# Optimization experiments

Measured on AMD Instinct MI355X. Metric: run time of the kernel, lower is better.

## Reference

```python
import jax, jax.numpy as jnp
import numpy as np

N_NODES = 20000
N_EDGES = 640000
H = 64            # node_hidden_size
E_FEAT = 16       # edge_features_size
T = 2             # num_prop_rounds


def setup_inputs() -> dict:
    key = jax.random.key(0)
    ks = jax.random.split(key, 10)
    hv = jax.random.normal(ks[0], (N_NODES, H), dtype=jnp.float32)
    e = jax.random.normal(ks[1], (N_EDGES, E_FEAT), dtype=jnp.float32)
    src = jax.random.randint(ks[2], (N_EDGES,), 0, N_NODES, dtype=jnp.int32)
    dst = jax.random.randint(ks[3], (N_EDGES,), 0, N_NODES, dtype=jnp.int32)
    s = 0.1  # param init scale to keep activations in a sane range
    W_msg = jax.random.normal(ks[4], (T, 2 * H + E_FEAT, 2 * H), dtype=jnp.float32) * s
    b_msg = jax.random.normal(ks[5], (T, 2 * H), dtype=jnp.float32) * s
    W_ih = jax.random.normal(ks[6], (T, 3 * H, 2 * H), dtype=jnp.float32) * s
    W_hh = jax.random.normal(ks[7], (T, 3 * H, H), dtype=jnp.float32) * s
    b_ih = jax.random.normal(ks[8], (T, 3 * H), dtype=jnp.float32) * s
    b_hh = jax.random.normal(ks[9], (T, 3 * H), dtype=jnp.float32) * s
    return {"hv": hv, "e": e, "src": src, "dst": dst,
            "W_msg": W_msg, "b_msg": b_msg,
            "W_ih": W_ih, "W_hh": W_hh, "b_ih": b_ih, "b_hh": b_hh}


def _gru_cell(a, h, W_ih, W_hh, b_ih, b_hh):
    # torch.nn.GRUCell math
    gi = a @ W_ih.T + b_ih   # [N, 3H]
    gh = h @ W_hh.T + b_hh   # [N, 3H]
    i_r, i_z, i_n = jnp.split(gi, 3, axis=1)
    h_r, h_z, h_n = jnp.split(gh, 3, axis=1)
    r = jax.nn.sigmoid(i_r + h_r)
    z = jax.nn.sigmoid(i_z + h_z)
    n = jnp.tanh(i_n + r * h_n)
    return (1.0 - z) * n + z * h


def reference(hv, e, src, dst, W_msg, b_msg, W_ih, W_hh, b_ih, b_hh):
    num_nodes = hv.shape[0]
    num_rounds = W_msg.shape[0]
    for t in range(num_rounds):  # small fixed loop over prop rounds
        # per-edge: concat([h_dst, h_src, e_uv]) -> Linear -> sum-reduce to dst
        msg_in = jnp.concatenate([hv[dst], hv[src], e], axis=1)  # [E, 2H+Ef]
        msgs = msg_in @ W_msg[t] + b_msg[t]                      # [E, 2H]
        a = jax.ops.segment_sum(msgs, dst, num_segments=num_nodes)  # [N, 2H]
        hv = _gru_cell(a, hv, W_ih[t], W_hh[t], b_ih[t], b_hh[t])
    return hv
```

## Files before the change

### kernel.cpp

```cpp
#include <hip/hip_runtime.h>
#include <cstddef>
#include <cstdint>

#define NN 20000
#define NE 640000
#define MP 20096
#define KA 224
#define NC 16
#define CHUNK 40000
#define NB_SCAN 79

typedef _Float16 f16x8 __attribute__((ext_vector_type(8)));
typedef float f32x4 __attribute__((ext_vector_type(4)));
typedef unsigned short u16x8 __attribute__((ext_vector_type(8)));

__device__ __forceinline__ float h2f(unsigned short u) {
    _Float16 h;
    *reinterpret_cast<unsigned short*>(&h) = u;
    return (float)h;
}
__device__ __forceinline__ unsigned short f2h(float f) {
    _Float16 h = (_Float16)f;
    return *reinterpret_cast<unsigned short*>(&h);
}
__device__ __forceinline__ void splitf(float x, unsigned short& hi, unsigned short& lo) {
    _Float16 h = (_Float16)x;
    _Float16 l = (_Float16)(x - (float)h);
    hi = *reinterpret_cast<unsigned short*>(&h);
    lo = *reinterpret_cast<unsigned short*>(&l);
}

__global__ void init_kernel(const float* __restrict__ hv0, unsigned short* __restrict__ hf0,
                            int* __restrict__ cnt) {
    int i = blockIdx.x * blockDim.x + threadIdx.x;
    if (i < NC * NN) cnt[i] = 0;
    if (i < NN * 64) hf0[i] = f2h(hv0[i]);
}

__global__ void hist_kernel(const int* __restrict__ dst, int* __restrict__ cnt) {
    int i = blockIdx.x * blockDim.x + threadIdx.x;
    if (i < NE) atomicAdd(&cnt[(i / CHUNK) * NN + dst[i]], 1);
}

__global__ __launch_bounds__(256) void scan1_kernel(const int* __restrict__ cnt,
                                                    int* __restrict__ lp,
                                                    int* __restrict__ bsum) {
    __shared__ int s[256];
    int t = threadIdx.x;
    int i = blockIdx.x * 256 + t;
    int d = 0;
    if (i < NN)
#pragma unroll
        for (int c = 0; c < NC; ++c) d += cnt[c * NN + i];
    s[t] = d;
    __syncthreads();
    for (int off = 1; off < 256; off <<= 1) {
        int v = (t >= off) ? s[t - off] : 0;
        __syncthreads();
        s[t] += v;
        __syncthreads();
    }
    if (i < NN) lp[i] = s[t] - d;
    if (t == 255) bsum[blockIdx.x] = s[255];
}

__global__ __launch_bounds__(256) void scan3_kernel(const int* __restrict__ cnt,
                                                    const int* __restrict__ lp,
                                                    const int* __restrict__ bsum,
                                                    int* __restrict__ row_ptr,
                                                    int* __restrict__ cursor) {
    __shared__ int sb[128];
    int t = threadIdx.x;
    if (t < 128) sb[t] = (t < NB_SCAN) ? bsum[t] : 0;
    __syncthreads();
    for (int off = 1; off < 128; off <<= 1) {
        int u = (t < 128 && t >= off) ? sb[t - off] : 0;
        __syncthreads();
        if (t < 128) sb[t] += u;
        __syncthreads();
    }
    int boff = (blockIdx.x == 0) ? 0 : sb[blockIdx.x - 1];
    int i = blockIdx.x * 256 + t;
    if (i < NN) {
        int run = boff + lp[i];
        row_ptr[i] = run;
#pragma unroll
        for (int c = 0; c < NC; ++c) {
            cursor[c * NN + i] = run;
            run += cnt[c * NN + i];
        }
    }
    if (i == 0) row_ptr[NN] = NE;
}

__global__ void place_kernel(const int* __restrict__ src, const int* __restrict__ dst,
                             int* __restrict__ cursor, int2* __restrict__ adj) {
    int i = blockIdx.x * blockDim.x + threadIdx.x;
    if (i < NE) {
        int d = dst[i];
        int pos = atomicAdd(&cursor[(i / CHUNK) * NN + d], 1);
        adj[pos] = make_int2(src[i], i);
    }
}

__global__ __launch_bounds__(256) void esum_csr_kernel(
        const float* __restrict__ ef, const int* __restrict__ row_ptr,
        const int2* __restrict__ adj, float* __restrict__ esum,
        float* __restrict__ degf) {
    int wid = threadIdx.x >> 6, lane = threadIdx.x & 63;
    int v = blockIdx.x * 4 + wid;
    if (v >= NN) return;
    int rp0 = row_ptr[v], rp1 = row_ptr[v + 1];
    int q = lane >> 2;
    int fo = (lane & 3) << 2;
    float4 a0 = make_float4(0.f, 0.f, 0.f, 0.f), a1 = a0;
    int i = rp0 + q;
    for (; i + 16 < rp1; i += 32) {
        int e0 = adj[i].y, e1 = adj[i + 16].y;
        float4 x0 = *(const float4*)(ef + (size_t)e0 * 16 + fo);
        float4 x1 = *(const float4*)(ef + (size_t)e1 * 16 + fo);
        a0.x += x0.x; a0.y += x0.y; a0.z += x0.z; a0.w += x0.w;
        a1.x += x1.x; a1.y += x1.y; a1.z += x1.z; a1.w += x1.w;
    }
    for (; i < rp1; i += 16) {
        int e = adj[i].y;
        float4 x = *(const float4*)(ef + (size_t)e * 16 + fo);
        a0.x += x.x; a0.y += x.y; a0.z += x.z; a0.w += x.w;
    }
    a0.x += a1.x; a0.y += a1.y; a0.z += a1.z; a0.w += a1.w;
#pragma unroll
    for (int m = 4; m < 64; m <<= 1) {
        a0.x += __shfl_xor(a0.x, m);
        a0.y += __shfl_xor(a0.y, m);
        a0.z += __shfl_xor(a0.z, m);
        a0.w += __shfl_xor(a0.w, m);
    }
    if (lane < 4) *(float4*)(esum + (size_t)v * 16 + fo) = a0;
    if (lane == 0) degf[v] = (float)(rp1 - rp0);
}

__global__ __launch_bounds__(192) void fold_kernel(
        const float* __restrict__ W_msg, const float* __restrict__ b_msg,
        const float* __restrict__ W_ih, const float* __restrict__ b_ih,
        const float* __restrict__ b_hh, const float* __restrict__ W_hh,
        unsigned short* __restrict__ Bhi, unsigned short* __restrict__ Blo) {
    if (blockIdx.x >= 18) {
        int aidx = (blockIdx.x - 18) * 192 + threadIdx.x;
        if (aidx >= 2 * 29504) return;
        int t = aidx / 29504, r = aidx % 29504;
        int n, k;
        if (r < 12288) { n = r >> 6; k = r & 63; }
        else if (r < 15168) { int q = r - 12288; n = q / 15; k = 209 + q % 15; }
        else { int q = r - 15168; n = 192 + q / 224; k = q % 224; }
        float v = 0.f;
        if (n < 192) {
            if (k < 64) {
                if (n < 128) v = W_hh[(size_t)t * 192 * 64 + n * 64 + k];
            } else if (k == 209) {
                v = (n < 128) ? (b_ih[t * 192 + n] + b_hh[t * 192 + n]) : b_ih[t * 192 + n];
            }
        } else {
            int j = n - 64;
            if (k < 64) v = W_hh[(size_t)t * 192 * 64 + j * 64 + k];
            else if (k == 209) v = b_hh[t * 192 + j];
        }
        unsigned short hi, lo;
        splitf(v, hi, lo);
        size_t o = ((size_t)t * 256 + n) * KA + k;
        Bhi[o] = hi;
        Blo[o] = lo;
        return;
    }
    __shared__ float ldsW[64][193];
    int t = blockIdx.x / 9;
    int k0 = (blockIdx.x % 9) * 16;
    int j = threadIdx.x;
    float acc[16];
#pragma unroll
    for (int kk = 0; kk < 16; ++kk) acc[kk] = 0.f;
    float bacc = 0.f;
    for (int mc = 0; mc < 2; ++mc) {
        for (int i = threadIdx.x; i < 192 * 64; i += 192) {
            int jj = i >> 6, mm = i & 63;
            ldsW[mm][jj] = W_ih[((size_t)t * 192 + jj) * 128 + mc * 64 + mm];
        }
        __syncthreads();
        for (int mm = 0; mm < 64; ++mm) {
            float wl = ldsW[mm][j];
            float bm = b_msg[t * 128 + mc * 64 + mm];
            bacc = fmaf(bm, wl, bacc);
#pragma unroll
            for (int kk = 0; kk < 16; ++kk) {
                float wm = W_msg[((size_t)t * 144 + k0 + kk) * 128 + mc * 64 + mm];
                acc[kk] = fmaf(wm, wl, acc[kk]);
            }
        }
        __syncthreads();
    }
    size_t rowo = ((size_t)t * 256 + j) * KA;
#pragma unroll
    for (int kk = 0; kk < 16; ++kk) {
        int kw = k0 + kk;
        int bcol = (kw < 64) ? (128 + kw) : ((kw < 128) ? kw : (64 + kw));
        unsigned short hi, lo;
        splitf(acc[kk], hi, lo);
        Bhi[rowo + bcol] = hi;
        Blo[rowo + bcol] = lo;
    }
    if (k0 == 0) {
        unsigned short hi, lo;
        splitf(bacc, hi, lo);
        Bhi[rowo + 208] = hi;
        Blo[rowo + 208] = lo;
    }
}

__global__ __launch_bounds__(256) void gather_kernel(
        const float* __restrict__ hv, const unsigned short* __restrict__ hf,
        const int* __restrict__ row_ptr, const int2* __restrict__ adj,
        const float* __restrict__ esum, const float* __restrict__ degf,
        unsigned short* __restrict__ Ahi, unsigned short* __restrict__ Alo) {
    int wid = threadIdx.x >> 6, lane = threadIdx.x & 63;
    int v = blockIdx.x * 4 + wid;
    if (v >= NN) return;
    int rp0 = row_ptr[v], rp1 = row_ptr[v + 1];
    int q = lane >> 3;
    int fo = (lane & 7) << 3;
    float a0[8], a1[8], a2[8], a3[8];
#pragma unroll
    for (int j = 0; j < 8; ++j) { a0[j] = 0.f; a1[j] = 0.f; a2[j] = 0.f; a3[j] = 0.f; }
    int i = rp0 + q;
    for (; i + 24 < rp1; i += 32) {
        int s0 = adj[i].x, s1 = adj[i + 8].x, s2 = adj[i + 16].x, s3 = adj[i + 24].x;
        u16x8 x0 = *(const u16x8*)(hf + (size_t)s0 * 64 + fo);
        u16x8 x1 = *(const u16x8*)(hf + (size_t)s1 * 64 + fo);
        u16x8 x2 = *(const u16x8*)(hf + (size_t)s2 * 64 + fo);
        u16x8 x3 = *(const u16x8*)(hf + (size_t)s3 * 64 + fo);
#pragma unroll
        for (int j = 0; j < 8; ++j) {
            a0[j] += h2f(x0[j]); a1[j] += h2f(x1[j]);
            a2[j] += h2f(x2[j]); a3[j] += h2f(x3[j]);
        }
    }
    for (; i < rp1; i += 8) {
        int s = adj[i].x;
        u16x8 x = *(const u16x8*)(hf + (size_t)s * 64 + fo);
#pragma unroll
        for (int j = 0; j < 8; ++j) a0[j] += h2f(x[j]);
    }
#pragma unroll
    for (int j = 0; j < 8; ++j) a0[j] += a1[j] + a2[j] + a3[j];
#pragma unroll
    for (int m = 8; m < 64; m <<= 1)
#pragma unroll
        for (int j = 0; j < 8; ++j) a0[j] += __shfl_xor(a0[j], m);
    if (lane < 8) {
        float dg = (float)(rp1 - rp0);
        float4 hA = *(const float4*)(hv + (size_t)v * 64 + lane * 8);
        float4 hB = *(const float4*)(hv + (size_t)v * 64 + lane * 8 + 4);
        float h8[8] = {hA.x, hA.y, hA.z, hA.w, hB.x, hB.y, hB.z, hB.w};
        u16x8 hh, sh, dh, dl;
#pragma unroll
        for (int j = 0; j < 8; ++j) {
            hh[j] = f2h(h8[j]);
            sh[j] = f2h(a0[j]);
            unsigned short thi, tlo;
            splitf(dg * h8[j], thi, tlo);
            dh[j] = thi; dl[j] = tlo;
        }
        *(u16x8*)(Ahi + (size_t)v * KA + fo) = hh;
        *(u16x8*)(Ahi + (size_t)v * KA + 64 + fo) = sh;
        *(u16x8*)(Ahi + (size_t)v * KA + 128 + fo) = dh;
        *(u16x8*)(Alo + (size_t)v * KA + 128 + fo) = dl;
    } else if (lane < 12) {
        int o = lane - 8;
        u16x8 tv;
#pragma unroll
        for (int j = 0; j < 8; ++j) tv[j] = 0;
        if (o < 2) {
#pragma unroll
            for (int j = 0; j < 8; ++j) tv[j] = f2h(esum[(size_t)v * 16 + o * 8 + j]);
        } else if (o == 2) {
            tv[0] = f2h(degf[v]);
            tv[1] = f2h(1.f);
        }
        *(u16x8*)(Ahi + (size_t)v * KA + 192 + o * 8) = tv;
    }
}

__global__ __launch_bounds__(256) void gemm_gru(
        const _Float16* __restrict__ Ahi, const _Float16* __restrict__ Alo,
        const _Float16* __restrict__ Bhi, const _Float16* __restrict__ Blo,
        const float* __restrict__ hin,
        float* __restrict__ fout, unsigned short* __restrict__ hfout) {
    __shared__ _Float16 Ash[64][40];
    __shared__ _Float16 Asl[64][40];
    __shared__ _Float16 Bsh[256][40];
    __shared__ _Float16 Bsl[256][40];
    int tid = threadIdx.x;
    int w = tid >> 6, l = tid & 63;
    int row0 = blockIdx.x * 64;
    f32x4 acc[16];
#pragma unroll
    for (int i = 0; i < 16; ++i) acc[i] = (f32x4){0.f, 0.f, 0.f, 0.f};

    int sAr = tid >> 2, sAc = (tid & 3) * 8;
    int kg = (l >> 4) * 8;
    int ar = w * 16 + (l & 15);
    int lc = l & 15;

#pragma unroll 1
    for (int ks = 0; ks < 2; ++ks) {
        int k0 = ks * 32;
        *(float4*)&Ash[sAr][sAc] = *(const float4*)(Ahi + (size_t)(row0 + sAr) * KA + k0 + sAc);
        {
            const float4* ph = (const float4*)(Bhi + (size_t)tid * KA + k0);
            float4 h0 = ph[0], h1 = ph[1], h2 = ph[2], h3 = ph[3];
            *(float4*)&Bsh[tid][0] = h0;  *(float4*)&Bsh[tid][8] = h1;
            *(float4*)&Bsh[tid][16] = h2; *(float4*)&Bsh[tid][24] = h3;
        }
        __syncthreads();
        f16x8 ah = *(const f16x8*)&Ash[ar][kg];
#pragma unroll
        for (int fn = 0; fn < 8; ++fn) {
            f16x8 bh = *(const f16x8*)&Bsh[fn * 16 + lc][kg];
            acc[fn] = __builtin_amdgcn_mfma_f32_16x16x32_f16(ah, bh, acc[fn], 0, 0, 0);
        }
#pragma unroll
        for (int fn = 12; fn < 16; ++fn) {
            f16x8 bh = *(const f16x8*)&Bsh[fn * 16 + lc][kg];
            acc[fn] = __builtin_amdgcn_mfma_f32_16x16x32_f16(ah, bh, acc[fn], 0, 0, 0);
        }
        __syncthreads();
    }

#pragma unroll 1
    for (int ks = 2; ks < 4; ++ks) {
        int k0 = ks * 32;
        *(float4*)&Ash[sAr][sAc] = *(const float4*)(Ahi + (size_t)(row0 + sAr) * KA + k0 + sAc);
        {
            const float4* ph = (const float4*)(Bhi + (size_t)tid * KA + k0);
            float4 h0 = ph[0], h1 = ph[1], h2 = ph[2], h3 = ph[3];
            *(float4*)&Bsh[tid][0] = h0;  *(float4*)&Bsh[tid][8] = h1;
            *(float4*)&Bsh[tid][16] = h2; *(float4*)&Bsh[tid][24] = h3;
        }
        __syncthreads();
        f16x8 ah = *(const f16x8*)&Ash[ar][kg];
#pragma unroll
        for (int fn = 0; fn < 12; ++fn) {
            f16x8 bh = *(const f16x8*)&Bsh[fn * 16 + lc][kg];
            acc[fn] = __builtin_amdgcn_mfma_f32_16x16x32_f16(ah, bh, acc[fn], 0, 0, 0);
        }
        __syncthreads();
    }

#pragma unroll 1
    for (int ks = 4; ks < 6; ++ks) {
        int k0 = ks * 32;
        *(float4*)&Ash[sAr][sAc] = *(const float4*)(Ahi + (size_t)(row0 + sAr) * KA + k0 + sAc);
        *(float4*)&Asl[sAr][sAc] = *(const float4*)(Alo + (size_t)(row0 + sAr) * KA + k0 + sAc);
        {
            const float4* ph = (const float4*)(Bhi + (size_t)tid * KA + k0);
            float4 h0 = ph[0], h1 = ph[1], h2 = ph[2], h3 = ph[3];
            *(float4*)&Bsh[tid][0] = h0;  *(float4*)&Bsh[tid][8] = h1;
            *(float4*)&Bsh[tid][16] = h2; *(float4*)&Bsh[tid][24] = h3;
            const float4* pl = (const float4*)(Blo + (size_t)tid * KA + k0);
            float4 l0 = pl[0], l1 = pl[1], l2 = pl[2], l3 = pl[3];
            *(float4*)&Bsl[tid][0] = l0;  *(float4*)&Bsl[tid][8] = l1;
            *(float4*)&Bsl[tid][16] = l2; *(float4*)&Bsl[tid][24] = l3;
        }
        __syncthreads();
        f16x8 ah = *(const f16x8*)&Ash[ar][kg];
        f16x8 al = *(const f16x8*)&Asl[ar][kg];
#pragma unroll
        for (int fn = 0; fn < 12; ++fn) {
            f16x8 bh = *(const f16x8*)&Bsh[fn * 16 + lc][kg];
            f16x8 bl = *(const f16x8*)&Bsl[fn * 16 + lc][kg];
            acc[fn] = __builtin_amdgcn_mfma_f32_16x16x32_f16(ah, bh, acc[fn], 0, 0, 0);
            acc[fn] = __builtin_amdgcn_mfma_f32_16x16x32_f16(ah, bl, acc[fn], 0, 0, 0);
            acc[fn] = __builtin_amdgcn_mfma_f32_16x16x32_f16(al, bh, acc[fn], 0, 0, 0);
        }
        __syncthreads();
    }

    {
        const int k0 = 192;
        *(float4*)&Ash[sAr][sAc] = *(const float4*)(Ahi + (size_t)(row0 + sAr) * KA + k0 + sAc);
        {
            const float4* ph = (const float4*)(Bhi + (size_t)tid * KA + k0);
            float4 h0 = ph[0], h1 = ph[1], h2 = ph[2], h3 = ph[3];
            *(float4*)&Bsh[tid][0] = h0;  *(float4*)&Bsh[tid][8] = h1;
            *(float4*)&Bsh[tid][16] = h2; *(float4*)&Bsh[tid][24] = h3;
            const float4* pl = (const float4*)(Blo + (size_t)tid * KA + k0);
            float4 l0 = pl[0], l1 = pl[1], l2 = pl[2], l3 = pl[3];
            *(float4*)&Bsl[tid][0] = l0;  *(float4*)&Bsl[tid][8] = l1;
            *(float4*)&Bsl[tid][16] = l2; *(float4*)&Bsl[tid][24] = l3;
        }
        __syncthreads();
        f16x8 ah = *(const f16x8*)&Ash[ar][kg];
#pragma unroll
        for (int fn = 0; fn < 16; ++fn) {
            f16x8 bh = *(const f16x8*)&Bsh[fn * 16 + lc][kg];
            f16x8 bl = *(const f16x8*)&Bsl[fn * 16 + lc][kg];
            acc[fn] = __builtin_amdgcn_mfma_f32_16x16x32_f16(ah, bh, acc[fn], 0, 0, 0);
            acc[fn] = __builtin_amdgcn_mfma_f32_16x16x32_f16(ah, bl, acc[fn], 0, 0, 0);
        }
        __syncthreads();
    }

    int jb = l & 15;
#pragma unroll
    for (int q = 0; q < 4; ++q) {
        int row = row0 + w * 16 + (l >> 4) * 4 + q;
        if (row >= NN) continue;
#pragma unroll
        for (int fj = 0; fj < 4; ++fj) {
            int j = jb + fj * 16;
            float rr = acc[fj][q];
            float zz = acc[4 + fj][q];
            float in_ = acc[8 + fj][q];
            float hn = acc[12 + fj][q];
            float r = 1.f / (1.f + __expf(-rr));
            float z = 1.f / (1.f + __expf(-zz));
            float n = tanhf(in_ + r * hn);
            float h = hin[(size_t)row * 64 + j];
            float val = (1.f - z) * n + z * h;
            fout[(size_t)row * 64 + j] = val;
            hfout[(size_t)row * 64 + j] = f2h(val);
        }
    }
}

extern "C" void kernel_launch(void* const* d_in, const int* in_sizes, int n_in,
                              void* d_out, int out_size, void* d_ws, size_t ws_size,
                              hipStream_t stream) {
    const float* hv0   = (const float*)d_in[0];
    const float* ef    = (const float*)d_in[1];
    const int*   src   = (const int*)d_in[2];
    const int*   dst   = (const int*)d_in[3];
    const float* W_msg = (const float*)d_in[4];
    const float* b_msg = (const float*)d_in[5];
    const float* W_ih  = (const float*)d_in[6];
    const float* W_hh  = (const float*)d_in[7];
    const float* b_ih  = (const float*)d_in[8];
    const float* b_hh  = (const float*)d_in[9];
    float* out = (float*)d_out;

    char* ws = (char*)d_ws;
    size_t off = 0;
    auto alloc = [&](size_t bytes) -> char* {
        char* p = ws + off;
        off = (off + bytes + 255) & ~(size_t)255;
        return p;
    };
    int*   cnt      = (int*)alloc((size_t)NC * NN * 4);
    int*   row_ptr  = (int*)alloc((NN + 1) * 4);
    int*   cursor   = (int*)alloc((size_t)NC * NN * 4);
    int2*  adj      = (int2*)alloc((size_t)NE * 8);
    float* esum     = (float*)alloc((size_t)NN * 16 * 4);
    float* degf     = (float*)alloc(NN * 4);
    int*   lp       = (int*)alloc(NN * 4);
    int*   bsum     = (int*)alloc(NB_SCAN * 4);
    unsigned short* Ahi = (unsigned short*)alloc((size_t)MP * KA * 2);
    unsigned short* Alo = (unsigned short*)alloc((size_t)MP * KA * 2);
    unsigned short* Bhi = (unsigned short*)alloc((size_t)2 * 256 * KA * 2);
    unsigned short* Blo = (unsigned short*)alloc((size_t)2 * 256 * KA * 2);
    float* hv1      = (float*)alloc((size_t)NN * 64 * 4);
    unsigned short* hf0 = (unsigned short*)alloc((size_t)NN * 64 * 2);
    unsigned short* hf1 = (unsigned short*)alloc((size_t)NN * 64 * 2);

    init_kernel<<<(NN * 64 + 255) / 256, 256, 0, stream>>>(hv0, hf0, cnt);
    hist_kernel<<<(NE + 255) / 256, 256, 0, stream>>>(dst, cnt);
    scan1_kernel<<<NB_SCAN, 256, 0, stream>>>(cnt, lp, bsum);
    scan3_kernel<<<NB_SCAN, 256, 0, stream>>>(cnt, lp, bsum, row_ptr, cursor);
    place_kernel<<<(NE + 255) / 256, 256, 0, stream>>>(src, dst, cursor, adj);
    esum_csr_kernel<<<(NN + 3) / 4, 256, 0, stream>>>(ef, row_ptr, adj, esum, degf);
    fold_kernel<<<18 + (2 * 29504 + 191) / 192, 192, 0, stream>>>(
        W_msg, b_msg, W_ih, b_ih, b_hh, W_hh, Bhi, Blo);

    for (int t = 0; t < 2; ++t) {
        const float* hin = (t == 0) ? hv0 : hv1;
        const unsigned short* hfin = (t == 0) ? hf0 : hf1;
        float* hout = (t == 1) ? out : hv1;
        gather_kernel<<<(NN + 3) / 4, 256, 0, stream>>>(hin, hfin, row_ptr, adj,
                                                        esum, degf, Ahi, Alo);
        gemm_gru<<<MP / 64, 256, 0, stream>>>(
            (const _Float16*)Ahi, (const _Float16*)Alo,
            (const _Float16*)(Bhi + (size_t)t * 256 * KA),
            (const _Float16*)(Blo + (size_t)t * 256 * KA),
            hin, hout, hf1);
    }
}
```

Baseline: 196.7 us.

## Merge init and weight-fold kernels; fuse edge-feature sum into first gather

```diff
diff --git a/kernel.cpp b/kernel.cpp
--- a/kernel.cpp
+++ b/kernel.cpp
@@ -13,6 +13,7 @@
 typedef _Float16 f16x8 __attribute__((ext_vector_type(8)));
 typedef float f32x4 __attribute__((ext_vector_type(4)));
 typedef unsigned short u16x8 __attribute__((ext_vector_type(8)));
+typedef unsigned short u16x4 __attribute__((ext_vector_type(4)));
 
 __device__ __forceinline__ float h2f(unsigned short u) {
     _Float16 h;
@@ -30,122 +31,22 @@
     lo = *reinterpret_cast<unsigned short*>(&l);
 }
 
-__global__ void init_kernel(const float* __restrict__ hv0, unsigned short* __restrict__ hf0,
-                            int* __restrict__ cnt) {
-    int i = blockIdx.x * blockDim.x + threadIdx.x;
-    if (i < NC * NN) cnt[i] = 0;
-    if (i < NN * 64) hf0[i] = f2h(hv0[i]);
-}
-
-__global__ void hist_kernel(const int* __restrict__ dst, int* __restrict__ cnt) {
-    int i = blockIdx.x * blockDim.x + threadIdx.x;
-    if (i < NE) atomicAdd(&cnt[(i / CHUNK) * NN + dst[i]], 1);
-}
-
-__global__ __launch_bounds__(256) void scan1_kernel(const int* __restrict__ cnt,
-                                                    int* __restrict__ lp,
-                                                    int* __restrict__ bsum) {
-    __shared__ int s[256];
-    int t = threadIdx.x;
-    int i = blockIdx.x * 256 + t;
-    int d = 0;
-    if (i < NN)
-#pragma unroll
-        for (int c = 0; c < NC; ++c) d += cnt[c * NN + i];
-    s[t] = d;
-    __syncthreads();
-    for (int off = 1; off < 256; off <<= 1) {
-        int v = (t >= off) ? s[t - off] : 0;
-        __syncthreads();
-        s[t] += v;
-        __syncthreads();
-    }
-    if (i < NN) lp[i] = s[t] - d;
-    if (t == 255) bsum[blockIdx.x] = s[255];
-}
-
-__global__ __launch_bounds__(256) void scan3_kernel(const int* __restrict__ cnt,
-                                                    const int* __restrict__ lp,
-                                                    const int* __restrict__ bsum,
-                                                    int* __restrict__ row_ptr,
-                                                    int* __restrict__ cursor) {
-    __shared__ int sb[128];
-    int t = threadIdx.x;
-    if (t < 128) sb[t] = (t < NB_SCAN) ? bsum[t] : 0;
-    __syncthreads();
-    for (int off = 1; off < 128; off <<= 1) {
-        int u = (t < 128 && t >= off) ? sb[t - off] : 0;
-        __syncthreads();
-        if (t < 128) sb[t] += u;
-        __syncthreads();
-    }
-    int boff = (blockIdx.x == 0) ? 0 : sb[blockIdx.x - 1];
-    int i = blockIdx.x * 256 + t;
-    if (i < NN) {
-        int run = boff + lp[i];
-        row_ptr[i] = run;
-#pragma unroll
-        for (int c = 0; c < NC; ++c) {
-            cursor[c * NN + i] = run;
-            run += cnt[c * NN + i];
-        }
-    }
-    if (i == 0) row_ptr[NN] = NE;
-}
-
-__global__ void place_kernel(const int* __restrict__ src, const int* __restrict__ dst,
-                             int* __restrict__ cursor, int2* __restrict__ adj) {
-    int i = blockIdx.x * blockDim.x + threadIdx.x;
-    if (i < NE) {
-        int d = dst[i];
-        int pos = atomicAdd(&cursor[(i / CHUNK) * NN + d], 1);
-        adj[pos] = make_int2(src[i], i);
-    }
-}
-
-__global__ __launch_bounds__(256) void esum_csr_kernel(
-        const float* __restrict__ ef, const int* __restrict__ row_ptr,
-        const int2* __restrict__ adj, float* __restrict__ esum,
-        float* __restrict__ degf) {
-    int wid = threadIdx.x >> 6, lane = threadIdx.x & 63;
-    int v = blockIdx.x * 4 + wid;
-    if (v >= NN) return;
-    int rp0 = row_ptr[v], rp1 = row_ptr[v + 1];
-    int q = lane >> 2;
-    int fo = (lane & 3) << 2;
-    float4 a0 = make_float4(0.f, 0.f, 0.f, 0.f), a1 = a0;
-    int i = rp0 + q;
-    for (; i + 16 < rp1; i += 32) {
-        int e0 = adj[i].y, e1 = adj[i + 16].y;
-        float4 x0 = *(const float4*)(ef + (size_t)e0 * 16 + fo);
-        float4 x1 = *(const float4*)(ef + (size_t)e1 * 16 + fo);
-        a0.x += x0.x; a0.y += x0.y; a0.z += x0.z; a0.w += x0.w;
-        a1.x += x1.x; a1.y += x1.y; a1.z += x1.z; a1.w += x1.w;
-    }
-    for (; i < rp1; i += 16) {
-        int e = adj[i].y;
-        float4 x = *(const float4*)(ef + (size_t)e * 16 + fo);
-        a0.x += x.x; a0.y += x.y; a0.z += x.z; a0.w += x.w;
-    }
-    a0.x += a1.x; a0.y += a1.y; a0.z += a1.z; a0.w += a1.w;
-#pragma unroll
-    for (int m = 4; m < 64; m <<= 1) {
-        a0.x += __shfl_xor(a0.x, m);
-        a0.y += __shfl_xor(a0.y, m);
-        a0.z += __shfl_xor(a0.z, m);
-        a0.w += __shfl_xor(a0.w, m);
-    }
-    if (lane < 4) *(float4*)(esum + (size_t)v * 16 + fo) = a0;
-    if (lane == 0) degf[v] = (float)(rp1 - rp0);
-}
-
-__global__ __launch_bounds__(192) void fold_kernel(
+__global__ __launch_bounds__(256) void prep_kernel(
+        const float* __restrict__ hv0, unsigned short* __restrict__ hf0,
+        int* __restrict__ cnt,
         const float* __restrict__ W_msg, const float* __restrict__ b_msg,
         const float* __restrict__ W_ih, const float* __restrict__ b_ih,
         const float* __restrict__ b_hh, const float* __restrict__ W_hh,
         unsigned short* __restrict__ Bhi, unsigned short* __restrict__ Blo) {
-    if (blockIdx.x >= 18) {
-        int aidx = (blockIdx.x - 18) * 192 + threadIdx.x;
+    int b = blockIdx.x;
+    if (b < 5000) {
+        int i = b * 256 + threadIdx.x;
+        if (i < NC * NN) cnt[i] = 0;
+        if (i < NN * 64) hf0[i] = f2h(hv0[i]);
+        return;
+    }
+    if (b >= 5018) {
+        int aidx = (b - 5018) * 256 + threadIdx.x;
         if (aidx >= 2 * 29504) return;
         int t = aidx / 29504, r = aidx % 29504;
         int n, k;
@@ -172,53 +73,125 @@
         return;
     }
     __shared__ float ldsW[64][193];
-    int t = blockIdx.x / 9;
-    int k0 = (blockIdx.x % 9) * 16;
+    int fb = b - 5000;
+    int t = fb / 9;
+    int k0 = (fb % 9) * 16;
     int j = threadIdx.x;
     float acc[16];
 #pragma unroll
     for (int kk = 0; kk < 16; ++kk) acc[kk] = 0.f;
     float bacc = 0.f;
     for (int mc = 0; mc < 2; ++mc) {
-        for (int i = threadIdx.x; i < 192 * 64; i += 192) {
+        for (int i = threadIdx.x; i < 192 * 64; i += 256) {
             int jj = i >> 6, mm = i & 63;
             ldsW[mm][jj] = W_ih[((size_t)t * 192 + jj) * 128 + mc * 64 + mm];
         }
         __syncthreads();
-        for (int mm = 0; mm < 64; ++mm) {
-            float wl = ldsW[mm][j];
-            float bm = b_msg[t * 128 + mc * 64 + mm];
-            bacc = fmaf(bm, wl, bacc);
-#pragma unroll
-            for (int kk = 0; kk < 16; ++kk) {
-                float wm = W_msg[((size_t)t * 144 + k0 + kk) * 128 + mc * 64 + mm];
-                acc[kk] = fmaf(wm, wl, acc[kk]);
+        if (j < 192) {
+            for (int mm = 0; mm < 64; ++mm) {
+                float wl = ldsW[mm][j];
+                float bm = b_msg[t * 128 + mc * 64 + mm];
+                bacc = fmaf(bm, wl, bacc);
+#pragma unroll
+                for (int kk = 0; kk < 16; ++kk) {
+                    float wm = W_msg[((size_t)t * 144 + k0 + kk) * 128 + mc * 64 + mm];
+                    acc[kk] = fmaf(wm, wl, acc[kk]);
+                }
             }
         }
         __syncthreads();
     }
-    size_t rowo = ((size_t)t * 256 + j) * KA;
-#pragma unroll
-    for (int kk = 0; kk < 16; ++kk) {
-        int kw = k0 + kk;
-        int bcol = (kw < 64) ? (128 + kw) : ((kw < 128) ? kw : (64 + kw));
-        unsigned short hi, lo;
-        splitf(acc[kk], hi, lo);
-        Bhi[rowo + bcol] = hi;
-        Blo[rowo + bcol] = lo;
-    }
-    if (k0 == 0) {
-        unsigned short hi, lo;
-        splitf(bacc, hi, lo);
-        Bhi[rowo + 208] = hi;
-        Blo[rowo + 208] = lo;
-    }
-}
-
+    if (j < 192) {
+        size_t rowo = ((size_t)t * 256 + j) * KA;
+#pragma unroll
+        for (int kk = 0; kk < 16; ++kk) {
+            int kw = k0 + kk;
+            int bcol = (kw < 64) ? (128 + kw) : ((kw < 128) ? kw : (64 + kw));
+            unsigned short hi, lo;
+            splitf(acc[kk], hi, lo);
+            Bhi[rowo + bcol] = hi;
+            Blo[rowo + bcol] = lo;
+        }
+        if (k0 == 0) {
+            unsigned short hi, lo;
+            splitf(bacc, hi, lo);
+            Bhi[rowo + 208] = hi;
+            Blo[rowo + 208] = lo;
+        }
+    }
+}
+
+__global__ void hist_kernel(const int* __restrict__ dst, int* __restrict__ cnt) {
+    int i = blockIdx.x * blockDim.x + threadIdx.x;
+    if (i < NE) atomicAdd(&cnt[(i / CHUNK) * NN + dst[i]], 1);
+}
+
+__global__ __launch_bounds__(256) void scan1_kernel(const int* __restrict__ cnt,
+                                                    int* __restrict__ lp,
+                                                    int* __restrict__ bsum) {
+    __shared__ int s[256];
+    int t = threadIdx.x;
+    int i = blockIdx.x * 256 + t;
+    int d = 0;
+    if (i < NN)
+#pragma unroll
+        for (int c = 0; c < NC; ++c) d += cnt[c * NN + i];
+    s[t] = d;
+    __syncthreads();
+    for (int off = 1; off < 256; off <<= 1) {
+        int v = (t >= off) ? s[t - off] : 0;
+        __syncthreads();
+        s[t] += v;
+        __syncthreads();
+    }
+    if (i < NN) lp[i] = s[t] - d;
+    if (t == 255) bsum[blockIdx.x] = s[255];
+}
+
+__global__ __launch_bounds__(256) void scan3_kernel(const int* __restrict__ cnt,
+                                                    const int* __restrict__ lp,
+                                                    const int* __restrict__ bsum,
+                                                    int* __restrict__ row_ptr,
+                                                    int* __restrict__ cursor) {
+    __shared__ int sb[128];
+    int t = threadIdx.x;
+    if (t < 128) sb[t] = (t < NB_SCAN) ? bsum[t] : 0;
+    __syncthreads();
+    for (int off = 1; off < 128; off <<= 1) {
+        int u = (t < 128 && t >= off) ? sb[t - off] : 0;
+        __syncthreads();
+        if (t < 128) sb[t] += u;
+        __syncthreads();
+    }
+    int boff = (blockIdx.x == 0) ? 0 : sb[blockIdx.x - 1];
+    int i = blockIdx.x * 256 + t;
+    if (i < NN) {
+        int run = boff + lp[i];
+        row_ptr[i] = run;
+#pragma unroll
+        for (int c = 0; c < NC; ++c) {
+            cursor[c * NN + i] = run;
+            run += cnt[c * NN + i];
+        }
+    }
+    if (i == 0) row_ptr[NN] = NE;
+}
+
+__global__ void place_kernel(const int* __restrict__ src, const int* __restrict__ dst,
+                             int* __restrict__ cursor, int2* __restrict__ adj) {
+    int i = blockIdx.x * blockDim.x + threadIdx.x;
+    if (i < NE) {
+        int d = dst[i];
+        int pos = atomicAdd(&cursor[(i / CHUNK) * NN + d], 1);
+        adj[pos] = make_int2(src[i], i);
+    }
+}
+
+template <bool FIRST>
 __global__ __launch_bounds__(256) void gather_kernel(
         const float* __restrict__ hv, const unsigned short* __restrict__ hf,
         const int* __restrict__ row_ptr, const int2* __restrict__ adj,
-        const float* __restrict__ esum, const float* __restrict__ degf,
+        const float* __restrict__ ef,
         unsigned short* __restrict__ Ahi, unsigned short* __restrict__ Alo) {
     int wid = threadIdx.x >> 6, lane = threadIdx.x & 63;
     int v = blockIdx.x * 4 + wid;
@@ -254,8 +227,8 @@
     for (int m = 8; m < 64; m <<= 1)
 #pragma unroll
         for (int j = 0; j < 8; ++j) a0[j] += __shfl_xor(a0[j], m);
+    float dg = (float)(rp1 - rp0);
     if (lane < 8) {
-        float dg = (float)(rp1 - rp0);
         float4 hA = *(const float4*)(hv + (size_t)v * 64 + lane * 8);
         float4 hB = *(const float4*)(hv + (size_t)v * 64 + lane * 8 + 4);
         float h8[8] = {hA.x, hA.y, hA.z, hA.w, hB.x, hB.y, hB.z, hB.w};
@@ -272,19 +245,40 @@
         *(u16x8*)(Ahi + (size_t)v * KA + 64 + fo) = sh;
         *(u16x8*)(Ahi + (size_t)v * KA + 128 + fo) = dh;
         *(u16x8*)(Alo + (size_t)v * KA + 128 + fo) = dl;
-    } else if (lane < 12) {
-        int o = lane - 8;
-        u16x8 tv;
-#pragma unroll
-        for (int j = 0; j < 8; ++j) tv[j] = 0;
-        if (o < 2) {
-#pragma unroll
-            for (int j = 0; j < 8; ++j) tv[j] = f2h(esum[(size_t)v * 16 + o * 8 + j]);
-        } else if (o == 2) {
-            tv[0] = f2h(degf[v]);
+    }
+    if (FIRST) {
+        int fo2 = (lane & 3) << 2;
+        float4 e = make_float4(0.f, 0.f, 0.f, 0.f);
+        for (int ii = rp0 + (lane >> 2); ii < rp1; ii += 16) {
+            int eid = adj[ii].y;
+            float4 x = *(const float4*)(ef + (size_t)eid * 16 + fo2);
+            e.x += x.x; e.y += x.y; e.z += x.z; e.w += x.w;
+        }
+#pragma unroll
+        for (int m = 4; m < 64; m <<= 1) {
+            e.x += __shfl_xor(e.x, m);
+            e.y += __shfl_xor(e.y, m);
+            e.z += __shfl_xor(e.z, m);
+            e.w += __shfl_xor(e.w, m);
+        }
+        if (lane < 4) {
+            u16x4 tv;
+            tv[0] = f2h(e.x); tv[1] = f2h(e.y);
+            tv[2] = f2h(e.z); tv[3] = f2h(e.w);
+            *(u16x4*)(Ahi + (size_t)v * KA + 192 + lane * 4) = tv;
+        } else if (lane == 4) {
+            u16x8 tv;
+#pragma unroll
+            for (int j = 0; j < 8; ++j) tv[j] = 0;
+            tv[0] = f2h(dg);
             tv[1] = f2h(1.f);
-        }
-        *(u16x8*)(Ahi + (size_t)v * KA + 192 + o * 8) = tv;
+            *(u16x8*)(Ahi + (size_t)v * KA + 208) = tv;
+        } else if (lane == 5) {
+            u16x8 tv;
+#pragma unroll
+            for (int j = 0; j < 8; ++j) tv[j] = 0;
+            *(u16x8*)(Ahi + (size_t)v * KA + 216) = tv;
+        }
     }
 }
 
@@ -457,8 +451,6 @@
     int*   row_ptr  = (int*)alloc((NN + 1) * 4);
     int*   cursor   = (int*)alloc((size_t)NC * NN * 4);
     int2*  adj      = (int2*)alloc((size_t)NE * 8);
-    float* esum     = (float*)alloc((size_t)NN * 16 * 4);
-    float* degf     = (float*)alloc(NN * 4);
     int*   lp       = (int*)alloc(NN * 4);
     int*   bsum     = (int*)alloc(NB_SCAN * 4);
     unsigned short* Ahi = (unsigned short*)alloc((size_t)MP * KA * 2);
@@ -469,25 +461,24 @@
     unsigned short* hf0 = (unsigned short*)alloc((size_t)NN * 64 * 2);
     unsigned short* hf1 = (unsigned short*)alloc((size_t)NN * 64 * 2);
 
-    init_kernel<<<(NN * 64 + 255) / 256, 256, 0, stream>>>(hv0, hf0, cnt);
+    prep_kernel<<<5000 + 18 + (2 * 29504 + 255) / 256, 256, 0, stream>>>(
+        hv0, hf0, cnt, W_msg, b_msg, W_ih, b_ih, b_hh, W_hh, Bhi, Blo);
     hist_kernel<<<(NE + 255) / 256, 256, 0, stream>>>(dst, cnt);
     scan1_kernel<<<NB_SCAN, 256, 0, stream>>>(cnt, lp, bsum);
     scan3_kernel<<<NB_SCAN, 256, 0, stream>>>(cnt, lp, bsum, row_ptr, cursor);
     place_kernel<<<(NE + 255) / 256, 256, 0, stream>>>(src, dst, cursor, adj);
-    esum_csr_kernel<<<(NN + 3) / 4, 256, 0, stream>>>(ef, row_ptr, adj, esum, degf);
-    fold_kernel<<<18 + (2 * 29504 + 191) / 192, 192, 0, stream>>>(
-        W_msg, b_msg, W_ih, b_ih, b_hh, W_hh, Bhi, Blo);
-
-    for (int t = 0; t < 2; ++t) {
-        const float* hin = (t == 0) ? hv0 : hv1;
-        const unsigned short* hfin = (t == 0) ? hf0 : hf1;
-        float* hout = (t == 1) ? out : hv1;
-        gather_kernel<<<(NN + 3) / 4, 256, 0, stream>>>(hin, hfin, row_ptr, adj,
-                                                        esum, degf, Ahi, Alo);
-        gemm_gru<<<MP / 64, 256, 0, stream>>>(
-            (const _Float16*)Ahi, (const _Float16*)Alo,
-            (const _Float16*)(Bhi + (size_t)t * 256 * KA),
-            (const _Float16*)(Blo + (size_t)t * 256 * KA),
-            hin, hout, hf1);
-    }
-}
+
+    gather_kernel<true><<<(NN + 3) / 4, 256, 0, stream>>>(
+        hv0, hf0, row_ptr, adj, ef, Ahi, Alo);
+    gemm_gru<<<MP / 64, 256, 0, stream>>>(
+        (const _Float16*)Ahi, (const _Float16*)Alo,
+        (const _Float16*)Bhi, (const _Float16*)Blo,
+        hv0, hv1, hf1);
+    gather_kernel<false><<<(NN + 3) / 4, 256, 0, stream>>>(
+        hv1, hf1, row_ptr, adj, ef, Ahi, Alo);
+    gemm_gru<<<MP / 64, 256, 0, stream>>>(
+        (const _Float16*)Ahi, (const _Float16*)Alo,
+        (const _Float16*)(Bhi + (size_t)256 * KA),
+        (const _Float16*)(Blo + (size_t)256 * KA),
+        hv1, out, hf1);
+}
```

Result: faster. 182.2 us (-7.4%).
